# Optimization experiments

Hardware: AMD Instinct MI355X
Metric: run time of the kernel (lower is better)

The kernel has to match this reference:

```python
import jax, jax.numpy as jnp
import numpy as np

B, T, C, HS = 8, 2048, 2048, 128  # batch, seq, n_embedding, head_size
THETA = 10000.0


def _rope_tables(dim, seq_len, theta=THETA):
    freqs = 1.0 / theta ** (jnp.arange(0, dim, 2, dtype=jnp.float32) / dim)  # [dim/2]
    t = jnp.arange(seq_len, dtype=jnp.float32)
    ang = jnp.outer(t, freqs)  # [T, dim/2]
    return jnp.cos(ang), jnp.sin(ang)


def _apply_rope(v, cos, sin):
    # v: [B,T,D]; pairs along last dim treated as complex (real=even, imag=odd)
    b, t, d = v.shape
    vr = v.reshape(b, t, d // 2, 2)
    x0, x1 = vr[..., 0], vr[..., 1]
    o0 = x0 * cos - x1 * sin
    o1 = x0 * sin + x1 * cos
    return jnp.stack([o0, o1], axis=-1).reshape(b, t, d)


def setup_inputs() -> dict:
    key = jax.random.key(0)
    k1, k2, k3, k4 = jax.random.split(key, 4)
    scale = 1.0 / np.sqrt(C)
    x = jax.random.normal(k1, (B, T, C), dtype=jnp.float32)
    Wk = jax.random.normal(k2, (C, HS), dtype=jnp.float32) * scale
    Wq = jax.random.normal(k3, (C, HS), dtype=jnp.float32) * scale
    Wv = jax.random.normal(k4, (C, HS), dtype=jnp.float32) * scale
    return {"x": x, "Wk": Wk, "Wq": Wq, "Wv": Wv}


def reference(x, Wk, Wq, Wv):
    b, t, _ = x.shape
    cos, sin = _rope_tables(HS, t)
    k = x @ Wk  # [B,T,HS]
    q = x @ Wq
    # Source: xq,xk = apply_rotary_emb(key, query); query,key = xq,xk
    # => scores = rope(q_proj) @ rope(k_proj)^T (standard causal attention)
    qr = _apply_rope(q, cos, sin)
    kr = _apply_rope(k, cos, sin)
    scores = jnp.einsum('btd,bsd->bts', qr, kr) * (HS ** -0.5)  # [B,T,T]
    causal = jnp.tril(jnp.ones((t, t), dtype=bool))
    scores = jnp.where(causal, scores, -jnp.inf)
    wei = jax.nn.softmax(scores, axis=-1)
    v = x @ Wv
    return jnp.einsum('bts,bsd->btd', wei, v)
```

## Files before the change

### kernel.cpp

```cpp
#include <hip/hip_runtime.h>

#define NB 8
#define NT 2048
#define NC 2048
#define NH 128

typedef short s8v __attribute__((ext_vector_type(8)));
typedef short s4v __attribute__((ext_vector_type(4)));
typedef float f4  __attribute__((ext_vector_type(4)));

static __device__ __forceinline__ unsigned short f2bf(float f) {
    union { float f; unsigned int u; } v; v.f = f;
    unsigned int x = v.u;
    return (unsigned short)((x + 0x7FFFu + ((x >> 16) & 1u)) >> 16);
}

static __device__ __forceinline__ s8v pack8(f4 lo, f4 hi) {
    union { f4 f; unsigned int u[4]; } L, H; L.f = lo; H.f = hi;
    union { s8v s; unsigned int u[4]; } A;
    A.u[0] = __builtin_amdgcn_perm(L.u[1], L.u[0], 0x07060302u);
    A.u[1] = __builtin_amdgcn_perm(L.u[3], L.u[2], 0x07060302u);
    A.u[2] = __builtin_amdgcn_perm(H.u[1], H.u[0], 0x07060302u);
    A.u[3] = __builtin_amdgcn_perm(H.u[3], H.u[2], 0x07060302u);
    return A.s;
}

__global__ __launch_bounds__(256) void wtrans_k(
    const float* __restrict__ Wk, const float* __restrict__ Wq,
    const float* __restrict__ Wv, unsigned short* __restrict__ wt)
{
    __shared__ float Ls[64][129];
    const int mat = blockIdx.y;
    const float* W = (mat == 0) ? Wq : (mat == 1) ? Wk : Wv;
    const int k0 = blockIdx.x * 64;
    const int t  = threadIdx.x;

    #pragma unroll
    for (int j = 0; j < 8; ++j) {
        int flat = j * 1024 + t * 4;
        int k = flat >> 7, n = flat & 127;
        f4 v = *reinterpret_cast<const f4*>(W + (size_t)(k0 + k) * NH + n);
        Ls[k][n] = v[0]; Ls[k][n + 1] = v[1]; Ls[k][n + 2] = v[2]; Ls[k][n + 3] = v[3];
    }
    __syncthreads();

    const int n = t >> 1, half = t & 1;
    unsigned short tmp[32];
    #pragma unroll
    for (int kk = 0; kk < 32; ++kk) tmp[kk] = f2bf(Ls[half * 32 + kk][n]);

    const int nb  = mat * 8 + (n >> 4);
    const int l16 = n & 15;
    const int kbi = blockIdx.x * 2 + half;
    unsigned short* dst = wt + ((size_t)nb * 64 + kbi) * 512;
    #pragma unroll
    for (int v = 0; v < 4; ++v)
        *reinterpret_cast<s8v*>(dst + (v * 16 + l16) * 8) = *reinterpret_cast<s8v*>(tmp + v * 8);
}

__global__ __launch_bounds__(512) void proj_rope(
    const float* __restrict__ x, const unsigned short* __restrict__ wt,
    unsigned short* __restrict__ qp, unsigned short* __restrict__ kp,
    unsigned short* __restrict__ vp)
{
    __shared__ char ALDS[2][9216];

    const int tid  = threadIdx.x;
    const int wave = tid >> 6;
    const int lane = tid & 63;
    const int quad = lane >> 4, l16 = lane & 15;
    const int wm = wave >> 2, wn = wave & 3;
    const int M0 = blockIdx.x * 64;

    const int srow = tid >> 3, sc = tid & 7;
    const float* xsrc = x + (size_t)(M0 + srow) * NC + sc * 8;
    char* sd0 = &ALDS[0][srow * 144 + sc * 16];
    char* sd1 = &ALDS[1][srow * 144 + sc * 16];

    const unsigned short* wtb = wt + (size_t)(wn * 6) * 32768 + lane * 8;

    f4 acc[2][6];
    #pragma unroll
    for (int mi = 0; mi < 2; ++mi)
        #pragma unroll
        for (int ni = 0; ni < 6; ++ni)
            acc[mi][ni] = (f4){0.f, 0.f, 0.f, 0.f};

    s8v bcur[2][6], bnxt[2][6];

    f4 a0lo = *reinterpret_cast<const f4*>(xsrc);
    f4 a0hi = *reinterpret_cast<const f4*>(xsrc + 4);
    f4 a1lo = *reinterpret_cast<const f4*>(xsrc + 64);
    f4 a1hi = *reinterpret_cast<const f4*>(xsrc + 68);
    #pragma unroll
    for (int ks = 0; ks < 2; ++ks)
        #pragma unroll
        for (int ni = 0; ni < 6; ++ni)
            bcur[ks][ni] = *reinterpret_cast<const s8v*>(wtb + (size_t)ni * 32768 + (size_t)ks * 512);
    *reinterpret_cast<s8v*>(sd0) = pack8(a0lo, a0hi);
    a0lo = *reinterpret_cast<const f4*>(xsrc + 128);
    a0hi = *reinterpret_cast<const f4*>(xsrc + 132);
    __syncthreads();

    for (int tt = 0; tt < 16; ++tt) {
        *reinterpret_cast<s8v*>(sd1) = pack8(a1lo, a1hi);
        if (tt < 15) {
            a1lo = *reinterpret_cast<const f4*>(xsrc + (size_t)(2 * tt + 3) * 64);
            a1hi = *reinterpret_cast<const f4*>(xsrc + (size_t)(2 * tt + 3) * 64 + 4);
        }
        #pragma unroll
        for (int ks = 0; ks < 2; ++ks)
            #pragma unroll
            for (int ni = 0; ni < 6; ++ni)
                bnxt[ks][ni] = *reinterpret_cast<const s8v*>(
                    wtb + (size_t)ni * 32768 + (size_t)((2 * tt + 1) * 2 + ks) * 512);
        #pragma unroll
        for (int ksub = 0; ksub < 2; ++ksub) {
            const char* cur = ALDS[0];
            s8v a0 = *reinterpret_cast<const s8v*>(cur + (wm * 32 + l16) * 144 + (ksub * 4 + quad) * 16);
            s8v a1 = *reinterpret_cast<const s8v*>(cur + (wm * 32 + 16 + l16) * 144 + (ksub * 4 + quad) * 16);
            #pragma unroll
            for (int ni = 0; ni < 6; ++ni) {
                acc[0][ni] = __builtin_amdgcn_mfma_f32_16x16x32_bf16(a0, bcur[ksub][ni], acc[0][ni], 0, 0, 0);
                acc[1][ni] = __builtin_amdgcn_mfma_f32_16x16x32_bf16(a1, bcur[ksub][ni], acc[1][ni], 0, 0, 0);
            }
        }
        __syncthreads();

        if (tt < 15) {
            *reinterpret_cast<s8v*>(sd0) = pack8(a0lo, a0hi);
            if (tt < 14) {
                a0lo = *reinterpret_cast<const f4*>(xsrc + (size_t)(2 * tt + 4) * 64);
                a0hi = *reinterpret_cast<const f4*>(xsrc + (size_t)(2 * tt + 4) * 64 + 4);
            }
            #pragma unroll
            for (int ks = 0; ks < 2; ++ks)
                #pragma unroll
                for (int ni = 0; ni < 6; ++ni)
                    bcur[ks][ni] = *reinterpret_cast<const s8v*>(
                        wtb + (size_t)ni * 32768 + (size_t)((2 * tt + 2) * 2 + ks) * 512);
        }
        #pragma unroll
        for (int ksub = 0; ksub < 2; ++ksub) {
            const char* cur = ALDS[1];
            s8v a0 = *reinterpret_cast<const s8v*>(cur + (wm * 32 + l16) * 144 + (ksub * 4 + quad) * 16);
            s8v a1 = *reinterpret_cast<const s8v*>(cur + (wm * 32 + 16 + l16) * 144 + (ksub * 4 + quad) * 16);
            #pragma unroll
            for (int ni = 0; ni < 6; ++ni) {
                acc[0][ni] = __builtin_amdgcn_mfma_f32_16x16x32_bf16(a0, bnxt[ksub][ni], acc[0][ni], 0, 0, 0);
                acc[1][ni] = __builtin_amdgcn_mfma_f32_16x16x32_bf16(a1, bnxt[ksub][ni], acc[1][ni], 0, 0, 0);
            }
        }
        __syncthreads();
    }

    const float cfreq = -0.10381025296f;
    const int tb  = M0 >> 11;
    const int tl  = M0 & 2047;
    unsigned short* qpB = qp + (size_t)tb * 262144;
    unsigned short* kpB = kp + (size_t)tb * 262144;
    unsigned short* vpB = vp + (size_t)tb * 262144;
    const int qt0 = (tl >> 5) + wm;
    const int kt0 = tl >> 6;

    #pragma unroll
    for (int mi = 0; mi < 2; ++mi) {
        #pragma unroll
        for (int ni = 0; ni < 6; ++ni) {
            const int outcol = wn * 96 + ni * 16 + l16;
            const int mat = outcol >> 7;
            const int col = outcol & 127;
            float vv[4];
            #pragma unroll
            for (int r = 0; r < 4; ++r) {
                const int t = tl + wm * 32 + mi * 16 + quad * 4 + r;
                float v = acc[mi][ni][r];
                if (mat < 2) {
                    float other = __shfl_xor(v, 1, 64);
                    float freq  = exp2f(cfreq * (float)(col & ~1));
                    float ang   = (float)t * freq;
                    float sn = sinf(ang), cs = cosf(ang);
                    v = (col & 1) ? (other * sn + v * cs)
                                  : (v * cs - other * sn);
                }
                vv[r] = v;
            }
            if (mat == 0) {
                const int ks = col >> 5, qq = (col >> 3) & 3, e = col & 7;
                unsigned short* d = qpB + ((((size_t)qt0 * 2 + mi) * 4 + ks) * 64 + qq * 16 + quad * 4) * 8 + e;
                #pragma unroll
                for (int r = 0; r < 4; ++r) d[r * 8] = f2bf(vv[r]);
            } else if (mat == 1) {
                const int ks = col >> 5, qq = (col >> 3) & 3, e = col & 7;
                const int nt = wm * 2 + mi;
                unsigned short* d = kpB + ((((size_t)kt0 * 4 + nt) * 4 + ks) * 64 + qq * 16 + quad * 4) * 8 + e;
                #pragma unroll
                for (int r = 0; r < 4; ++r) d[r * 8] = f2bf(vv[r]);
            } else {
                const int dt  = col >> 4;
                const int ks2 = wm;
                const int qv  = mi * 2 + (quad >> 1);
                const int e4  = (quad & 1) * 4;
                unsigned short* d = vpB + ((((size_t)kt0 * 2 + ks2) * 8 + dt) * 64 + qv * 16 + l16) * 8 + e4;
                s4v pk;
                #pragma unroll
                for (int r = 0; r < 4; ++r) pk[r] = (short)f2bf(vv[r]);
                *reinterpret_cast<s4v*>(d) = pk;
            }
        }
    }
}

__global__ __launch_bounds__(256, 2) void attn_k(
    const unsigned short* __restrict__ qp, const unsigned short* __restrict__ kp,
    const unsigned short* __restrict__ vp, float* __restrict__ out)
{
    __shared__ unsigned short P[4][32 * 64];
    __shared__ float Os[4][32][64];
    __shared__ float Ms[4][32], Ls[4][32], Lt[32];

    const int wave = threadIdx.x >> 6;
    const int lane = threadIdx.x & 63;
    const int quad = lane >> 4, l16 = lane & 15;
    const int b     = blockIdx.y;
    const int qrow0 = blockIdx.x * 32;
    const int qt    = blockIdx.x;
    const unsigned short* Qp = qp + (size_t)b * 262144;
    const unsigned short* Kp = kp + (size_t)b * 262144;
    const unsigned short* Vp = vp + (size_t)b * 262144;

    s8v qf[2][4];
    #pragma unroll
    for (int mi = 0; mi < 2; ++mi)
        #pragma unroll
        for (int ks = 0; ks < 4; ++ks)
            qf[mi][ks] = *reinterpret_cast<const s8v*>(
                Qp + ((((size_t)qt * 2 + mi) * 4 + ks) * 64 + lane) * 8);

    float m[2][4], ls[2][4];
    f4 o[2][8];
    #pragma unroll
    for (int mi = 0; mi < 2; ++mi) {
        #pragma unroll
        for (int r = 0; r < 4; ++r) { m[mi][r] = -INFINITY; ls[mi][r] = 0.f; }
        #pragma unroll
        for (int dt = 0; dt < 8; ++dt) o[mi][dt] = (f4){0.f, 0.f, 0.f, 0.f};
    }

    const int nkt = (qrow0 >> 6) + 1;
    const float scale2 = 0.1275166948f;

    for (int kt = wave; kt < nkt; kt += 4) {
        const int kbase = kt * 64;
        const bool domask = (kt == nkt - 1);
        const unsigned short* Kt = Kp + (size_t)kt * 8192;
        const unsigned short* Vt = Vp + (size_t)kt * 8192;

        f4 s[2][4];
        #pragma unroll
        for (int nt = 0; nt < 4; ++nt) {
            f4 a0 = (f4){0.f, 0.f, 0.f, 0.f}, a1 = a0;
            #pragma unroll
            for (int ks = 0; ks < 4; ++ks) {
                s8v kf = *reinterpret_cast<const s8v*>(Kt + (((nt * 4 + ks) * 64) + lane) * 8);
                a0 = __builtin_amdgcn_mfma_f32_16x16x32_bf16(qf[0][ks], kf, a0, 0, 0, 0);
                a1 = __builtin_amdgcn_mfma_f32_16x16x32_bf16(qf[1][ks], kf, a1, 0, 0, 0);
            }
            s[0][nt] = a0; s[1][nt] = a1;
        }

        float tmx[2][4];
        #pragma unroll
        for (int mi = 0; mi < 2; ++mi) {
            #pragma unroll
            for (int r = 0; r < 4; ++r) {
                const int trow = qrow0 + mi * 16 + quad * 4 + r;
                #pragma unroll
                for (int nt = 0; nt < 4; ++nt) {
                    float sv = s[mi][nt][r] * scale2;
                    if (domask && (kbase + nt * 16 + l16 > trow)) sv = -INFINITY;
                    s[mi][nt][r] = sv;
                }
                float tm = fmaxf(fmaxf(s[mi][0][r], s[mi][1][r]),
                                 fmaxf(s[mi][2][r], s[mi][3][r]));
                #pragma unroll
                for (int off = 1; off < 16; off <<= 1)
                    tm = fmaxf(tm, __shfl_xor(tm, off, 64));
                tmx[mi][r] = tm;
            }
        }

        bool grow = false;
        #pragma unroll
        for (int mi = 0; mi < 2; ++mi)
            #pragma unroll
            for (int r = 0; r < 4; ++r)
                grow = grow || (tmx[mi][r] > m[mi][r] + 8.0f);
        if (__any(grow)) {
            #pragma unroll
            for (int mi = 0; mi < 2; ++mi)
                #pragma unroll
                for (int r = 0; r < 4; ++r) {
                    const float mn = fmaxf(m[mi][r], tmx[mi][r]);
                    const float alpha = exp2f(m[mi][r] - mn);
                    m[mi][r] = mn;
                    ls[mi][r] *= alpha;
                    #pragma unroll
                    for (int dt = 0; dt < 8; ++dt) o[mi][dt][r] *= alpha;
                }
        }

        #pragma unroll
        for (int mi = 0; mi < 2; ++mi)
            #pragma unroll
            for (int r = 0; r < 4; ++r) {
                float rs = 0.f;
                #pragma unroll
                for (int nt = 0; nt < 4; ++nt) {
                    float p = exp2f(s[mi][nt][r] - m[mi][r]);
                    s[mi][nt][r] = p;
                    rs += p;
                }
                ls[mi][r] += rs;
            }

        #pragma unroll
        for (int mi = 0; mi < 2; ++mi)
            #pragma unroll
            for (int nt = 0; nt < 4; ++nt)
                #pragma unroll
                for (int r = 0; r < 4; ++r) {
                    const int prow = mi * 16 + quad * 4 + r;
                    const int swz  = ((nt * 2 + (l16 >> 3)) ^ (prow & 7)) * 8 + (l16 & 7);
                    P[wave][prow * 64 + swz] = f2bf(s[mi][nt][r]);
                }

        #pragma unroll
        for (int ks2 = 0; ks2 < 2; ++ks2) {
            s8v pa[2];
            #pragma unroll
            for (int mi = 0; mi < 2; ++mi) {
                const int prow = mi * 16 + l16;
                const int pp = ((ks2 * 4 + quad) ^ (l16 & 7));
                pa[mi] = *reinterpret_cast<const s8v*>(&P[wave][prow * 64 + pp * 8]);
            }
            #pragma unroll
            for (int dt = 0; dt < 8; ++dt) {
                s8v vf = *reinterpret_cast<const s8v*>(Vt + (((ks2 * 8 + dt) * 64) + lane) * 8);
                o[0][dt] = __builtin_amdgcn_mfma_f32_16x16x32_bf16(pa[0], vf, o[0][dt], 0, 0, 0);
                o[1][dt] = __builtin_amdgcn_mfma_f32_16x16x32_bf16(pa[1], vf, o[1][dt], 0, 0, 0);
            }
        }
    }

    #pragma unroll
    for (int mi = 0; mi < 2; ++mi)
        #pragma unroll
        for (int r = 0; r < 4; ++r) {
            float v = ls[mi][r];
            #pragma unroll
            for (int off = 1; off < 16; off <<= 1) v += __shfl_xor(v, off, 64);
            ls[mi][r] = v;
        }

    if (l16 == 0) {
        #pragma unroll
        for (int mi = 0; mi < 2; ++mi)
            #pragma unroll
            for (int r = 0; r < 4; ++r) {
                Ms[wave][mi * 16 + quad * 4 + r] = m[mi][r];
                Ls[wave][mi * 16 + quad * 4 + r] = ls[mi][r];
            }
    }
    __syncthreads();

    #pragma unroll
    for (int mi = 0; mi < 2; ++mi)
        #pragma unroll
        for (int r = 0; r < 4; ++r) {
            const int row = mi * 16 + quad * 4 + r;
            float M = fmaxf(fmaxf(Ms[0][row], Ms[1][row]), fmaxf(Ms[2][row], Ms[3][row]));
            float sc = exp2f(m[mi][r] - M);
            float lt = Ls[0][row] * exp2f(Ms[0][row] - M) + Ls[1][row] * exp2f(Ms[1][row] - M)
                     + Ls[2][row] * exp2f(Ms[2][row] - M) + Ls[3][row] * exp2f(Ms[3][row] - M);
            if (wave == 0 && l16 == 0) Lt[row] = lt;
            #pragma unroll
            for (int dt = 0; dt < 8; ++dt) o[mi][dt][r] *= sc;
        }

    const int rrow = threadIdx.x >> 3;
    const int cx   = (threadIdx.x & 7) * 8;
    #pragma unroll
    for (int h = 0; h < 2; ++h) {
        __syncthreads();
        #pragma unroll
        for (int mi = 0; mi < 2; ++mi)
            #pragma unroll
            for (int dtl = 0; dtl < 4; ++dtl)
                #pragma unroll
                for (int r = 0; r < 4; ++r)
                    Os[wave][mi * 16 + quad * 4 + r][dtl * 16 + l16] = o[mi][h * 4 + dtl][r];
        __syncthreads();
        f4 s0 = (f4){0.f, 0.f, 0.f, 0.f}, s1 = s0;
        #pragma unroll
        for (int w = 0; w < 4; ++w) {
            s0 += *reinterpret_cast<const f4*>(&Os[w][rrow][cx]);
            s1 += *reinterpret_cast<const f4*>(&Os[w][rrow][cx + 4]);
        }
        const float rl = 1.0f / Lt[rrow];
        float* dst = &out[((size_t)b * NT + qrow0 + rrow) * NH + h * 64 + cx];
        *reinterpret_cast<f4*>(dst)     = s0 * rl;
        *reinterpret_cast<f4*>(dst + 4) = s1 * rl;
    }
}

extern "C" void kernel_launch(void* const* d_in, const int* in_sizes, int n_in,
                              void* d_out, int out_size, void* d_ws, size_t ws_size,
                              hipStream_t stream) {
    const float* x  = (const float*)d_in[0];
    const float* Wk = (const float*)d_in[1];
    const float* Wq = (const float*)d_in[2];
    const float* Wv = (const float*)d_in[3];
    unsigned short* ws   = (unsigned short*)d_ws;
    unsigned short* wt   = ws;
    unsigned short* qws  = ws  + 786432;
    unsigned short* kws  = qws + 2097152;
    unsigned short* vtws = kws + 2097152;
    float* outp = (float*)d_out;

    wtrans_k<<<dim3(32, 3), 256, 0, stream>>>(Wk, Wq, Wv, wt);
    proj_rope<<<dim3(256), 512, 0, stream>>>(x, wt, qws, kws, vtws);
    attn_k<<<dim3(64, 8), 256, 0, stream>>>(qws, kws, vtws, outp);
}
```

Before: 285.3 us.

## Double proj_rope waves per block and alias attention LDS buffers for occupancy

proj_rope now launches 1024 threads per block, 16 waves instead of 8. Each wave computes half as many output columns, and each thread stages four fp32 values of x into LDS instead of eight. The attention kernel overlays its P tile buffer and its Os output staging buffer in one shared-memory allocation. That cuts LDS use so launch bounds can ask for 4 blocks per CU instead of 2. The aim is more latency hiding in the projection and higher attention occupancy, at the cost of tighter register budgets and reliance on barriers to make the LDS aliasing safe.

```diff
diff --git a/kernel.cpp b/kernel.cpp
--- a/kernel.cpp
+++ b/kernel.cpp
@@ -15,14 +15,12 @@
     return (unsigned short)((x + 0x7FFFu + ((x >> 16) & 1u)) >> 16);
 }
 
-static __device__ __forceinline__ s8v pack8(f4 lo, f4 hi) {
-    union { f4 f; unsigned int u[4]; } L, H; L.f = lo; H.f = hi;
-    union { s8v s; unsigned int u[4]; } A;
-    A.u[0] = __builtin_amdgcn_perm(L.u[1], L.u[0], 0x07060302u);
-    A.u[1] = __builtin_amdgcn_perm(L.u[3], L.u[2], 0x07060302u);
-    A.u[2] = __builtin_amdgcn_perm(H.u[1], H.u[0], 0x07060302u);
-    A.u[3] = __builtin_amdgcn_perm(H.u[3], H.u[2], 0x07060302u);
-    return A.s;
+static __device__ __forceinline__ void pack4st(f4 v, char* dst) {
+    union { f4 f; unsigned int u[4]; } V; V.f = v;
+    uint2 p;
+    p.x = __builtin_amdgcn_perm(V.u[1], V.u[0], 0x07060302u);
+    p.y = __builtin_amdgcn_perm(V.u[3], V.u[2], 0x07060302u);
+    *reinterpret_cast<uint2*>(dst) = p;
 }
 
 __global__ __launch_bounds__(256) void wtrans_k(
@@ -58,7 +56,7 @@
         *reinterpret_cast<s8v*>(dst + (v * 16 + l16) * 8) = *reinterpret_cast<s8v*>(tmp + v * 8);
 }
 
-__global__ __launch_bounds__(512) void proj_rope(
+__global__ __launch_bounds__(1024, 4) void proj_rope(
     const float* __restrict__ x, const unsigned short* __restrict__ wt,
     unsigned short* __restrict__ qp, unsigned short* __restrict__ kp,
     unsigned short* __restrict__ vp)
@@ -69,86 +67,81 @@
     const int wave = tid >> 6;
     const int lane = tid & 63;
     const int quad = lane >> 4, l16 = lane & 15;
-    const int wm = wave >> 2, wn = wave & 3;
+    const int wm = wave >> 3, wn = wave & 7;
     const int M0 = blockIdx.x * 64;
 
-    const int srow = tid >> 3, sc = tid & 7;
-    const float* xsrc = x + (size_t)(M0 + srow) * NC + sc * 8;
-    char* sd0 = &ALDS[0][srow * 144 + sc * 16];
-    char* sd1 = &ALDS[1][srow * 144 + sc * 16];
-
-    const unsigned short* wtb = wt + (size_t)(wn * 6) * 32768 + lane * 8;
-
-    f4 acc[2][6];
+    const int srow = tid >> 4, sc = tid & 15;
+    const float* xsrc = x + (size_t)(M0 + srow) * NC + sc * 4;
+    char* sd0 = &ALDS[0][srow * 144 + sc * 8];
+    char* sd1 = &ALDS[1][srow * 144 + sc * 8];
+
+    const unsigned short* wtb = wt + (size_t)(wn * 3) * 32768 + lane * 8;
+
+    f4 acc[2][3];
     #pragma unroll
     for (int mi = 0; mi < 2; ++mi)
         #pragma unroll
-        for (int ni = 0; ni < 6; ++ni)
+        for (int ni = 0; ni < 3; ++ni)
             acc[mi][ni] = (f4){0.f, 0.f, 0.f, 0.f};
 
-    s8v bcur[2][6], bnxt[2][6];
-
-    f4 a0lo = *reinterpret_cast<const f4*>(xsrc);
-    f4 a0hi = *reinterpret_cast<const f4*>(xsrc + 4);
-    f4 a1lo = *reinterpret_cast<const f4*>(xsrc + 64);
-    f4 a1hi = *reinterpret_cast<const f4*>(xsrc + 68);
+    s8v bcur[2][3], bnxt[2][3];
+
+    f4 a0 = *reinterpret_cast<const f4*>(xsrc);
+    f4 a1 = *reinterpret_cast<const f4*>(xsrc + 64);
     #pragma unroll
     for (int ks = 0; ks < 2; ++ks)
         #pragma unroll
-        for (int ni = 0; ni < 6; ++ni)
+        for (int ni = 0; ni < 3; ++ni)
             bcur[ks][ni] = *reinterpret_cast<const s8v*>(wtb + (size_t)ni * 32768 + (size_t)ks * 512);
-    *reinterpret_cast<s8v*>(sd0) = pack8(a0lo, a0hi);
-    a0lo = *reinterpret_cast<const f4*>(xsrc + 128);
-    a0hi = *reinterpret_cast<const f4*>(xsrc + 132);
+    pack4st(a0, sd0);
+    a0 = *reinterpret_cast<const f4*>(xsrc + 128);
     __syncthreads();
 
     for (int tt = 0; tt < 16; ++tt) {
-        *reinterpret_cast<s8v*>(sd1) = pack8(a1lo, a1hi);
+        pack4st(a1, sd1);
         if (tt < 15) {
-            a1lo = *reinterpret_cast<const f4*>(xsrc + (size_t)(2 * tt + 3) * 64);
-            a1hi = *reinterpret_cast<const f4*>(xsrc + (size_t)(2 * tt + 3) * 64 + 4);
+            a1 = *reinterpret_cast<const f4*>(xsrc + (size_t)(2 * tt + 3) * 64);
         }
         #pragma unroll
         for (int ks = 0; ks < 2; ++ks)
             #pragma unroll
-            for (int ni = 0; ni < 6; ++ni)
+            for (int ni = 0; ni < 3; ++ni)
                 bnxt[ks][ni] = *reinterpret_cast<const s8v*>(
                     wtb + (size_t)ni * 32768 + (size_t)((2 * tt + 1) * 2 + ks) * 512);
         #pragma unroll
         for (int ksub = 0; ksub < 2; ++ksub) {
             const char* cur = ALDS[0];
-            s8v a0 = *reinterpret_cast<const s8v*>(cur + (wm * 32 + l16) * 144 + (ksub * 4 + quad) * 16);
-            s8v a1 = *reinterpret_cast<const s8v*>(cur + (wm * 32 + 16 + l16) * 144 + (ksub * 4 + quad) * 16);
-            #pragma unroll
-            for (int ni = 0; ni < 6; ++ni) {
-                acc[0][ni] = __builtin_amdgcn_mfma_f32_16x16x32_bf16(a0, bcur[ksub][ni], acc[0][ni], 0, 0, 0);
-                acc[1][ni] = __builtin_amdgcn_mfma_f32_16x16x32_bf16(a1, bcur[ksub][ni], acc[1][ni], 0, 0, 0);
+            s8v av0 = *reinterpret_cast<const s8v*>(cur + (wm * 32 + l16) * 144 + (ksub * 4 + quad) * 16);
+            s8v av1 = *reinterpret_cast<const s8v*>(cur + (wm * 32 + 16 + l16) * 144 + (ksub * 4 + quad) * 16);
+            #pragma unroll
+            for (int ni = 0; ni < 3; ++ni) {
+                acc[0][ni] = __builtin_amdgcn_mfma_f32_16x16x32_bf16(av0, bcur[ksub][ni], acc[0][ni], 0, 0, 0);
+                acc[1][ni] = __builtin_amdgcn_mfma_f32_16x16x32_bf16(av1, bcur[ksub][ni], acc[1][ni], 0, 0, 0);
             }
         }
         __syncthreads();
 
         if (tt < 15) {
-            *reinterpret_cast<s8v*>(sd0) = pack8(a0lo, a0hi);
+            pack4st(a0, sd0);
             if (tt < 14) {
-                a0lo = *reinterpret_cast<const f4*>(xsrc + (size_t)(2 * tt + 4) * 64);
-                a0hi = *reinterpret_cast<const f4*>(xsrc + (size_t)(2 * tt + 4) * 64 + 4);
+                a0 = *reinterpret_cast<const f4*>(xsrc + (size_t)(2 * tt + 4) * 64);
             }
             #pragma unroll
             for (int ks = 0; ks < 2; ++ks)
                 #pragma unroll
-                for (int ni = 0; ni < 6; ++ni)
+                for (int ni = 0; ni < 3; ++ni)
                     bcur[ks][ni] = *reinterpret_cast<const s8v*>(
                         wtb + (size_t)ni * 32768 + (size_t)((2 * tt + 2) * 2 + ks) * 512);
         }
         #pragma unroll
         for (int ksub = 0; ksub < 2; ++ksub) {
             const char* cur = ALDS[1];
-            s8v a0 = *reinterpret_cast<const s8v*>(cur + (wm * 32 + l16) * 144 + (ksub * 4 + quad) * 16);
-            s8v a1 = *reinterpret_cast<const s8v*>(cur + (wm * 32 + 16 + l16) * 144 + (ksub * 4 + quad) * 16);
-            #pragma unroll
-            for (int ni = 0; ni < 6; ++ni) {
-                acc[0][ni] = __builtin_amdgcn_mfma_f32_16x16x32_bf16(a0, bnxt[ksub][ni], acc[0][ni], 0, 0, 0);
-                acc[1][ni] = __builtin_amdgcn_mfma_f32_16x16x32_bf16(a1, bnxt[ksub][ni], acc[1][ni], 0, 0, 0);
+            s8v av0 = *reinterpret_cast<const s8v*>(cur + (wm * 32 + l16) * 144 + (ksub * 4 + quad) * 16);
+            s8v av1 = *reinterpret_cast<const s8v*>(cur + (wm * 32 + 16 + l16) * 144 + (ksub * 4 + quad) * 16);
+            #pragma unroll
+            for (int ni = 0; ni < 3; ++ni) {
+                acc[0][ni] = __builtin_amdgcn_mfma_f32_16x16x32_bf16(av0, bnxt[ksub][ni], acc[0][ni], 0, 0, 0);
+                acc[1][ni] = __builtin_amdgcn_mfma_f32_16x16x32_bf16(av1, bnxt[ksub][ni], acc[1][ni], 0, 0, 0);
             }
         }
         __syncthreads();
@@ -166,8 +159,8 @@
     #pragma unroll
     for (int mi = 0; mi < 2; ++mi) {
         #pragma unroll
-        for (int ni = 0; ni < 6; ++ni) {
-            const int outcol = wn * 96 + ni * 16 + l16;
+        for (int ni = 0; ni < 3; ++ni) {
+            const int outcol = wn * 48 + ni * 16 + l16;
             const int mat = outcol >> 7;
             const int col = outcol & 127;
             float vv[4];
@@ -211,13 +204,16 @@
     }
 }
 
-__global__ __launch_bounds__(256, 2) void attn_k(
+__global__ __launch_bounds__(256, 4) void attn_k(
     const unsigned short* __restrict__ qp, const unsigned short* __restrict__ kp,
     const unsigned short* __restrict__ vp, float* __restrict__ out)
 {
-    __shared__ unsigned short P[4][32 * 64];
-    __shared__ float Os[4][32][64];
-    __shared__ float Ms[4][32], Ls[4][32], Lt[32];
+    __shared__ __align__(16) char SMEM[33920];
+    auto* P  = reinterpret_cast<unsigned short(*)[2048]>(SMEM);
+    auto* Os = reinterpret_cast<float(*)[32][64]>(SMEM);
+    float* MsF = reinterpret_cast<float*>(SMEM + 32768);
+    float* LsF = reinterpret_cast<float*>(SMEM + 33280);
+    float* Lt  = reinterpret_cast<float*>(SMEM + 33792);
 
     const int wave = threadIdx.x >> 6;
     const int lane = threadIdx.x & 63;
@@ -368,8 +364,8 @@
         for (int mi = 0; mi < 2; ++mi)
             #pragma unroll
             for (int r = 0; r < 4; ++r) {
-                Ms[wave][mi * 16 + quad * 4 + r] = m[mi][r];
-                Ls[wave][mi * 16 + quad * 4 + r] = ls[mi][r];
+                MsF[wave * 32 + mi * 16 + quad * 4 + r] = m[mi][r];
+                LsF[wave * 32 + mi * 16 + quad * 4 + r] = ls[mi][r];
             }
     }
     __syncthreads();
@@ -379,10 +375,10 @@
         #pragma unroll
         for (int r = 0; r < 4; ++r) {
             const int row = mi * 16 + quad * 4 + r;
-            float M = fmaxf(fmaxf(Ms[0][row], Ms[1][row]), fmaxf(Ms[2][row], Ms[3][row]));
+            float M = fmaxf(fmaxf(MsF[row], MsF[32 + row]), fmaxf(MsF[64 + row], MsF[96 + row]));
             float sc = exp2f(m[mi][r] - M);
-            float lt = Ls[0][row] * exp2f(Ms[0][row] - M) + Ls[1][row] * exp2f(Ms[1][row] - M)
-                     + Ls[2][row] * exp2f(Ms[2][row] - M) + Ls[3][row] * exp2f(Ms[3][row] - M);
+            float lt = LsF[row] * exp2f(MsF[row] - M) + LsF[32 + row] * exp2f(MsF[32 + row] - M)
+                     + LsF[64 + row] * exp2f(MsF[64 + row] - M) + LsF[96 + row] * exp2f(MsF[96 + row] - M);
             if (wave == 0 && l16 == 0) Lt[row] = lt;
             #pragma unroll
             for (int dt = 0; dt < 8; ++dt) o[mi][dt][r] *= sc;
@@ -429,6 +425,6 @@
     float* outp = (float*)d_out;
 
     wtrans_k<<<dim3(32, 3), 256, 0, stream>>>(Wk, Wq, Wv, wt);
-    proj_rope<<<dim3(256), 512, 0, stream>>>(x, wt, qws, kws, vtws);
+    proj_rope<<<dim3(256), 1024, 0, stream>>>(x, wt, qws, kws, vtws);
     attn_k<<<dim3(64, 8), 256, 0, stream>>>(qws, kws, vtws, outp);
 }
```

Result: slower. 428.6 us (+50.2%).

## Use direct global-to-LDS loads for x in projection and remap waves to columns

Applied to the files above, without the earlier changes.

The projection kernel now streams fp32 x tiles straight into LDS with global_load_lds in an XOR-swizzled layout, and converts to bf16 when each wave reads from LDS, so the register staging and bf16 pack before the LDS store are gone. The wave tiling changes from a 2x4 grid (32 rows x 96 cols per wave) to each wave owning all 64 rows and 48 columns. The B-fragment register double-buffering is dropped for a single-buffered LDS ping-pong with one barrier per k-step. The costs are twice the LDS footprint (fp32 instead of bf16), the conversion repeated by every wave, and less prefetch depth for the weight loads.

```diff
diff --git a/kernel.cpp b/kernel.cpp
--- a/kernel.cpp
+++ b/kernel.cpp
@@ -23,6 +23,12 @@
     A.u[2] = __builtin_amdgcn_perm(H.u[1], H.u[0], 0x07060302u);
     A.u[3] = __builtin_amdgcn_perm(H.u[3], H.u[2], 0x07060302u);
     return A.s;
+}
+
+static __device__ __forceinline__ void gl2lds16(const void* g, void* lds_base) {
+    __builtin_amdgcn_global_load_lds(
+        (const __attribute__((address_space(1))) unsigned int*)g,
+        (__attribute__((address_space(3))) unsigned int*)lds_base, 16, 0, 0);
 }
 
 __global__ __launch_bounds__(256) void wtrans_k(
@@ -63,117 +69,89 @@
     unsigned short* __restrict__ qp, unsigned short* __restrict__ kp,
     unsigned short* __restrict__ vp)
 {
-    __shared__ char ALDS[2][9216];
+    __shared__ float Xs[2][4096];
 
     const int tid  = threadIdx.x;
     const int wave = tid >> 6;
     const int lane = tid & 63;
     const int quad = lane >> 4, l16 = lane & 15;
-    const int wm = wave >> 2, wn = wave & 3;
     const int M0 = blockIdx.x * 64;
 
-    const int srow = tid >> 3, sc = tid & 7;
-    const float* xsrc = x + (size_t)(M0 + srow) * NC + sc * 8;
-    char* sd0 = &ALDS[0][srow * 144 + sc * 16];
-    char* sd1 = &ALDS[1][srow * 144 + sc * 16];
-
-    const unsigned short* wtb = wt + (size_t)(wn * 6) * 32768 + lane * 8;
-
-    f4 acc[2][6];
-    #pragma unroll
-    for (int mi = 0; mi < 2; ++mi)
-        #pragma unroll
-        for (int ni = 0; ni < 6; ++ni)
+    const float* xsrc[2];
+    #pragma unroll
+    for (int s = 0; s < 2; ++s) {
+        const int xrow = wave * 8 + s * 4 + (lane >> 4);
+        const int xcol = ((lane & 15) ^ (xrow & 15)) * 4;
+        xsrc[s] = x + (size_t)(M0 + xrow) * NC + xcol;
+    }
+
+    const unsigned short* wtb = wt + (size_t)(wave * 3) * 32768 + lane * 8;
+
+    f4 acc[4][3];
+    #pragma unroll
+    for (int mi = 0; mi < 4; ++mi)
+        #pragma unroll
+        for (int ni = 0; ni < 3; ++ni)
             acc[mi][ni] = (f4){0.f, 0.f, 0.f, 0.f};
 
-    s8v bcur[2][6], bnxt[2][6];
-
-    f4 a0lo = *reinterpret_cast<const f4*>(xsrc);
-    f4 a0hi = *reinterpret_cast<const f4*>(xsrc + 4);
-    f4 a1lo = *reinterpret_cast<const f4*>(xsrc + 64);
-    f4 a1hi = *reinterpret_cast<const f4*>(xsrc + 68);
-    #pragma unroll
-    for (int ks = 0; ks < 2; ++ks)
-        #pragma unroll
-        for (int ni = 0; ni < 6; ++ni)
-            bcur[ks][ni] = *reinterpret_cast<const s8v*>(wtb + (size_t)ni * 32768 + (size_t)ks * 512);
-    *reinterpret_cast<s8v*>(sd0) = pack8(a0lo, a0hi);
-    a0lo = *reinterpret_cast<const f4*>(xsrc + 128);
-    a0hi = *reinterpret_cast<const f4*>(xsrc + 132);
+    #pragma unroll
+    for (int s = 0; s < 2; ++s)
+        gl2lds16(xsrc[s], (char*)Xs[0] + (wave * 2 + s) * 1024);
     __syncthreads();
 
-    for (int tt = 0; tt < 16; ++tt) {
-        *reinterpret_cast<s8v*>(sd1) = pack8(a1lo, a1hi);
-        if (tt < 15) {
-            a1lo = *reinterpret_cast<const f4*>(xsrc + (size_t)(2 * tt + 3) * 64);
-            a1hi = *reinterpret_cast<const f4*>(xsrc + (size_t)(2 * tt + 3) * 64 + 4);
-        }
+    for (int t = 0; t < 32; ++t) {
+        s8v b[2][3];
         #pragma unroll
         for (int ks = 0; ks < 2; ++ks)
             #pragma unroll
-            for (int ni = 0; ni < 6; ++ni)
-                bnxt[ks][ni] = *reinterpret_cast<const s8v*>(
-                    wtb + (size_t)ni * 32768 + (size_t)((2 * tt + 1) * 2 + ks) * 512);
+            for (int ni = 0; ni < 3; ++ni)
+                b[ks][ni] = *reinterpret_cast<const s8v*>(
+                    wtb + (size_t)ni * 32768 + (size_t)(t * 2 + ks) * 512);
+        if (t < 31) {
+            #pragma unroll
+            for (int s = 0; s < 2; ++s)
+                gl2lds16(xsrc[s] + (t + 1) * 64, (char*)Xs[(t + 1) & 1] + (wave * 2 + s) * 1024);
+        }
+        const float* cur = Xs[t & 1];
         #pragma unroll
         for (int ksub = 0; ksub < 2; ++ksub) {
-            const char* cur = ALDS[0];
-            s8v a0 = *reinterpret_cast<const s8v*>(cur + (wm * 32 + l16) * 144 + (ksub * 4 + quad) * 16);
-            s8v a1 = *reinterpret_cast<const s8v*>(cur + (wm * 32 + 16 + l16) * 144 + (ksub * 4 + quad) * 16);
-            #pragma unroll
-            for (int ni = 0; ni < 6; ++ni) {
-                acc[0][ni] = __builtin_amdgcn_mfma_f32_16x16x32_bf16(a0, bcur[ksub][ni], acc[0][ni], 0, 0, 0);
-                acc[1][ni] = __builtin_amdgcn_mfma_f32_16x16x32_bf16(a1, bcur[ksub][ni], acc[1][ni], 0, 0, 0);
-            }
+            s8v a[4];
+            #pragma unroll
+            for (int mi = 0; mi < 4; ++mi) {
+                const int rb = (mi * 16 + l16) * 64;
+                const int p0 = (ksub * 8 + quad * 2) ^ l16;
+                f4 L = *reinterpret_cast<const f4*>(cur + rb + p0 * 4);
+                f4 H = *reinterpret_cast<const f4*>(cur + rb + (p0 ^ 1) * 4);
+                a[mi] = pack8(L, H);
+            }
+            #pragma unroll
+            for (int ni = 0; ni < 3; ++ni)
+                #pragma unroll
+                for (int mi = 0; mi < 4; ++mi)
+                    acc[mi][ni] = __builtin_amdgcn_mfma_f32_16x16x32_bf16(a[mi], b[ksub][ni], acc[mi][ni], 0, 0, 0);
         }
         __syncthreads();
-
-        if (tt < 15) {
-            *reinterpret_cast<s8v*>(sd0) = pack8(a0lo, a0hi);
-            if (tt < 14) {
-                a0lo = *reinterpret_cast<const f4*>(xsrc + (size_t)(2 * tt + 4) * 64);
-                a0hi = *reinterpret_cast<const f4*>(xsrc + (size_t)(2 * tt + 4) * 64 + 4);
-            }
-            #pragma unroll
-            for (int ks = 0; ks < 2; ++ks)
-                #pragma unroll
-                for (int ni = 0; ni < 6; ++ni)
-                    bcur[ks][ni] = *reinterpret_cast<const s8v*>(
-                        wtb + (size_t)ni * 32768 + (size_t)((2 * tt + 2) * 2 + ks) * 512);
-        }
-        #pragma unroll
-        for (int ksub = 0; ksub < 2; ++ksub) {
-            const char* cur = ALDS[1];
-            s8v a0 = *reinterpret_cast<const s8v*>(cur + (wm * 32 + l16) * 144 + (ksub * 4 + quad) * 16);
-            s8v a1 = *reinterpret_cast<const s8v*>(cur + (wm * 32 + 16 + l16) * 144 + (ksub * 4 + quad) * 16);
-            #pragma unroll
-            for (int ni = 0; ni < 6; ++ni) {
-                acc[0][ni] = __builtin_amdgcn_mfma_f32_16x16x32_bf16(a0, bnxt[ksub][ni], acc[0][ni], 0, 0, 0);
-                acc[1][ni] = __builtin_amdgcn_mfma_f32_16x16x32_bf16(a1, bnxt[ksub][ni], acc[1][ni], 0, 0, 0);
-            }
-        }
-        __syncthreads();
     }
 
     const float cfreq = -0.10381025296f;
-    const int tb  = M0 >> 11;
-    const int tl  = M0 & 2047;
+    const int tb = M0 >> 11;
+    const int tl = M0 & 2047;
     unsigned short* qpB = qp + (size_t)tb * 262144;
     unsigned short* kpB = kp + (size_t)tb * 262144;
     unsigned short* vpB = vp + (size_t)tb * 262144;
-    const int qt0 = (tl >> 5) + wm;
     const int kt0 = tl >> 6;
 
     #pragma unroll
-    for (int mi = 0; mi < 2; ++mi) {
-        #pragma unroll
-        for (int ni = 0; ni < 6; ++ni) {
-            const int outcol = wn * 96 + ni * 16 + l16;
+    for (int mi = 0; mi < 4; ++mi) {
+        #pragma unroll
+        for (int ni = 0; ni < 3; ++ni) {
+            const int outcol = wave * 48 + ni * 16 + l16;
             const int mat = outcol >> 7;
             const int col = outcol & 127;
             float vv[4];
             #pragma unroll
             for (int r = 0; r < 4; ++r) {
-                const int t = tl + wm * 32 + mi * 16 + quad * 4 + r;
+                const int t = tl + mi * 16 + quad * 4 + r;
                 float v = acc[mi][ni][r];
                 if (mat < 2) {
                     float other = __shfl_xor(v, 1, 64);
@@ -186,20 +164,20 @@
                 vv[r] = v;
             }
             if (mat == 0) {
+                const int qt = (tl >> 5) + (mi >> 1);
                 const int ks = col >> 5, qq = (col >> 3) & 3, e = col & 7;
-                unsigned short* d = qpB + ((((size_t)qt0 * 2 + mi) * 4 + ks) * 64 + qq * 16 + quad * 4) * 8 + e;
+                unsigned short* d = qpB + ((((size_t)qt * 2 + (mi & 1)) * 4 + ks) * 64 + qq * 16 + quad * 4) * 8 + e;
                 #pragma unroll
                 for (int r = 0; r < 4; ++r) d[r * 8] = f2bf(vv[r]);
             } else if (mat == 1) {
                 const int ks = col >> 5, qq = (col >> 3) & 3, e = col & 7;
-                const int nt = wm * 2 + mi;
-                unsigned short* d = kpB + ((((size_t)kt0 * 4 + nt) * 4 + ks) * 64 + qq * 16 + quad * 4) * 8 + e;
+                unsigned short* d = kpB + ((((size_t)kt0 * 4 + mi) * 4 + ks) * 64 + qq * 16 + quad * 4) * 8 + e;
                 #pragma unroll
                 for (int r = 0; r < 4; ++r) d[r * 8] = f2bf(vv[r]);
             } else {
                 const int dt  = col >> 4;
-                const int ks2 = wm;
-                const int qv  = mi * 2 + (quad >> 1);
+                const int ks2 = mi >> 1;
+                const int qv  = (mi & 1) * 2 + (quad >> 1);
                 const int e4  = (quad & 1) * 4;
                 unsigned short* d = vpB + ((((size_t)kt0 * 2 + ks2) * 8 + dt) * 64 + qv * 16 + l16) * 8 + e4;
                 s4v pk;
```

New measurement: 295.9 us. 1.04x slower.
